# Performance work log

Measured on AMD Instinct MI355X. Metric: run time of the kernel, lower is better.

The kernel has to match this reference:

```python
import jax, jax.numpy as jnp
import numpy as np

BASE_R = 0.1      # base_radius (compared against squared distances)
K = 20            # PositionEncoder k
H = 0.1           # dilated_ball_query bandwidth
EPS_BN = 1e-5


def _gelu(x):
    return jax.nn.gelu(x, approximate=False)  # torch nn.GELU default (erf)


def _bn(x, g, b):
    # eval-mode BatchNorm (running_mean=0, running_var=1), channel axis = 1
    shape = (1, -1) + (1,) * (x.ndim - 2)
    scale = g / np.float32(np.sqrt(1.0 + EPS_BN))
    return x * scale.reshape(shape) + b.reshape(shape)


def _conv1x1(x, w):
    # pointwise conv (no bias): w [out_c, in_c], x [B, in_c, ...]
    return jnp.einsum('oc,bc...->bo...', w, x)


def _l1norm(x, axis):
    # F.normalize(p=1): divide by L1 norm clamped to 1e-12
    return x / jnp.maximum(jnp.sum(jnp.abs(x), axis=axis, keepdims=True), 1e-12)


def _forward(xyz, w_q, g_q, b_q, w_k, g_k, b_k, w_v, g_v, b_v,
             w_pe, b_pe, g_pe, bb_pe, w_m1, g_m1, b_m1, w_m2, g_m2, b_m2,
             w_out, g_out, b_out):
    B, _, N = xyz.shape
    # ---- pairwise squared distances [B,N,N] ----
    sq = jnp.sum(xyz * xyz, axis=1)
    dist = -2.0 * jnp.einsum('bcn,bcm->bnm', xyz, xyz) + sq[:, :, None] + sq[:, None, :]
    # ---- dilated ball query (sigma=1) ----
    gauss = jnp.exp(-dist / (2.0 * H * H))
    kd = jnp.sum(gauss, axis=-1, keepdims=True)                 # [B,N,1]
    kd_score = kd / (jnp.max(kd, axis=1, keepdims=True) + 1e-9)
    radius = BASE_R + BASE_R * kd_score                         # max_radius = 2*base
    keep = dist < radius                                        # [B,N,N]
    # ---- masked attention (emb_cent == emb_x == cat(xyz, xyz)) ----
    emb = jnp.concatenate([xyz, xyz], axis=1)                   # [B,6,N]
    q = _bn(_conv1x1(emb, w_q), g_q, b_q)                       # [B,1,N]
    k_ = _bn(_conv1x1(emb, w_k), g_k, b_k)                      # [B,1,N]
    scores = jnp.einsum('bhn,bhm->bnm', q, k_)                  # [B,N,N]
    scores = jnp.where(keep, scores, -1e9)
    adj = jax.nn.softmax(scores, axis=-1)
    adj = _l1norm(_l1norm(adj, 1), -1)                          # doubly L1-normalized
    # ---- graph smoothing + value conv ----
    smoothed = jnp.einsum('bcn,bnm->bcm', xyz, adj)
    variation = smoothed - xyz
    v = _bn(_conv1x1(jnp.concatenate([variation, xyz], axis=1), w_v), g_v, b_v)  # [B,64,N]
    # ---- position encoder: ball-query top-k neighbor gather ----
    ar = jnp.arange(N, dtype=jnp.int32)[None, None, :]
    idx = jnp.where(dist > radius, N, ar)                       # mark out-of-ball with N
    idx = jnp.sort(idx, axis=-1)[:, :, :K]                      # k nearest-index in-ball
    idx = jnp.where(idx == N, idx[:, :, :1], idx)               # pad with first neighbor
    grouped = jax.vmap(lambda f, i: f[:, i])(xyz, idx)          # [B,3,N,K]
    pts = jnp.broadcast_to(xyz[:, :, :, None], grouped.shape)
    pf = jnp.concatenate([pts, grouped, grouped - pts], axis=1)  # [B,9,N,K]
    pf = _conv1x1(pf, w_pe) + b_pe[None, :, None, None]          # conv2d 1x1 with bias
    pf = _gelu(_bn(pf, g_pe, bb_pe))
    pf = jnp.max(pf, axis=-1)                                    # [B,out/8,N]
    pf = _gelu(_bn(_conv1x1(pf, w_m1), g_m1, b_m1))              # [B,out/4,N]
    pos = _bn(_conv1x1(pf, w_m2), g_m2, b_m2)                    # [B,out,N]
    out = _gelu(v + pos)
    return _bn(_conv1x1(out, w_out), g_out, b_out)               # [B,32,N]


def setup_inputs() -> dict:
    key = jax.random.key(0)
    ks = iter(jax.random.split(key, 40))
    B, N, OC = 4, 4096, 64

    def w(shape):
        return jax.random.normal(next(ks), shape, jnp.float32) / np.float32(np.sqrt(shape[-1]))

    def gb(c):
        g = 1.0 + 0.1 * jax.random.normal(next(ks), (c,), jnp.float32)
        b = 0.1 * jax.random.normal(next(ks), (c,), jnp.float32)
        return g, b

    xyz = jax.random.uniform(next(ks), (B, 3, N), jnp.float32)
    g_q, b_q = gb(1)
    g_k, b_k = gb(1)
    g_v, b_v = gb(OC)
    g_pe, bb_pe = gb(OC // 8)
    g_m1, b_m1 = gb(OC // 4)
    g_m2, b_m2 = gb(OC)
    g_out, b_out = gb(32)
    return {
        'xyz': xyz,
        'w_q': w((1, 6)), 'g_q': g_q, 'b_q': b_q,
        'w_k': w((1, 6)), 'g_k': g_k, 'b_k': b_k,
        'w_v': w((OC, 6)), 'g_v': g_v, 'b_v': b_v,
        'w_pe': w((OC // 8, 9)), 'b_pe': 0.1 * jax.random.normal(next(ks), (OC // 8,), jnp.float32),
        'g_pe': g_pe, 'bb_pe': bb_pe,
        'w_m1': w((OC // 4, OC // 8)), 'g_m1': g_m1, 'b_m1': b_m1,
        'w_m2': w((OC, OC // 4)), 'g_m2': g_m2, 'b_m2': b_m2,
        'w_out': w((32, OC)), 'g_out': g_out, 'b_out': b_out,
    }


def reference(xyz, w_q, g_q, b_q, w_k, g_k, b_k, w_v, g_v, b_v,
              w_pe, b_pe, g_pe, bb_pe, w_m1, g_m1, b_m1, w_m2, g_m2, b_m2,
              w_out, g_out, b_out):
    return _forward(xyz, w_q, g_q, b_q, w_k, g_k, b_k, w_v, g_v, b_v,
                    w_pe, b_pe, g_pe, bb_pe, w_m1, g_m1, b_m1, w_m2, g_m2, b_m2,
                    w_out, g_out, b_out)
```

## Files before the change

kernel.cpp:

```cpp
#include <hip/hip_runtime.h>
#include <math.h>

#define BB 4
#define NN 4096
#define KNBR 20
#define BN (BB * NN)
#define HALF 2048
#define RPW 128

__device__ __forceinline__ float gelu_f(float x) {
    return 0.5f * x * (1.0f + erff(x * 0.70710678118654752440f));
}

__global__ void k0_prep(const float* __restrict__ xyz,
                        const float* __restrict__ w_q, const float* __restrict__ g_q, const float* __restrict__ b_q,
                        const float* __restrict__ w_k, const float* __restrict__ g_k, const float* __restrict__ b_k,
                        float* __restrict__ qv, float* __restrict__ kv, float4* __restrict__ pts4) {
    int t = blockIdx.x * blockDim.x + threadIdx.x;
    if (t >= BN) return;
    int b = t / NN, n = t % NN;
    const float* base = xyz + (size_t)b * 3 * NN;
    float x = base[n], y = base[NN + n], z = base[2 * NN + n];
    float sq = x * x + y * y + z * z;
    const float invs = rsqrtf(1.0f + 1e-5f);
    float qr = x * (w_q[0] + w_q[3]) + y * (w_q[1] + w_q[4]) + z * (w_q[2] + w_q[5]);
    float kr = x * (w_k[0] + w_k[3]) + y * (w_k[1] + w_k[4]) + z * (w_k[2] + w_k[5]);
    qv[t] = qr * (g_q[0] * invs) + b_q[0];
    kv[t] = kr * (g_k[0] * invs) + b_k[0];
    pts4[t] = make_float4(x, y, z, sq);
}

__global__ __launch_bounds__(1024, 8)
void p1_kd(const float4* __restrict__ pts4, float* __restrict__ part) {
    int tid = threadIdx.x;
    int wave = __builtin_amdgcn_readfirstlane(tid >> 6);
    int lane = tid & 63;
    int g = blockIdx.x >> 1, half = blockIdx.x & 1;
    int b = g >> 6;
    const float4* p = pts4 + (size_t)b * NN;
    float4 fr = pts4[g * 64 + lane];
    float acc = 0.f;
    int i0 = half * HALF + wave * RPW;
    for (int i = i0; i < i0 + RPW; i += 8) {
        float4 fc[8];
        #pragma unroll
        for (int u = 0; u < 8; ++u) fc[u] = p[i + u];
        #pragma unroll
        for (int u = 0; u < 8; ++u) {
            float dot = fr.x * fc[u].x + fr.y * fc[u].y + fr.z * fc[u].z;
            float d = fmaf(-2.0f, dot, fr.w) + fc[u].w;
            acc += __expf(-50.0f * d);
        }
    }
    __shared__ float s_red[16][64];
    s_red[wave][lane] = acc;
    __syncthreads();
    if (tid < 64) {
        float s = 0.f;
        #pragma unroll
        for (int w = 0; w < 16; ++w) s += s_red[w][tid];
        part[half * BN + g * 64 + tid] = s;
    }
}

__global__ void k2_radius(const float* __restrict__ part, const float4* __restrict__ pts4,
                          const float* __restrict__ qv, const float* __restrict__ kv,
                          float* __restrict__ radius, float4* __restrict__ recB) {
    int b = blockIdx.x;
    int t = threadIdx.x;
    float kdv[4];
    float mx = -1e30f;
    #pragma unroll
    for (int j = 0; j < 4; ++j) {
        int n = b * NN + j * 1024 + t;
        kdv[j] = part[n] + part[BN + n];
        mx = fmaxf(mx, kdv[j]);
    }
    __shared__ float red[1024];
    red[t] = mx;
    __syncthreads();
    for (int s = 512; s > 0; s >>= 1) {
        if (t < s) red[t] = fmaxf(red[t], red[t + s]);
        __syncthreads();
    }
    float kmax = red[0];
    #pragma unroll
    for (int j = 0; j < 4; ++j) {
        int n = b * NN + j * 1024 + t;
        float rad = 0.1f + 0.1f * (kdv[j] / (kmax + 1e-9f));
        radius[n] = rad;
        recB[2 * n] = pts4[n];
        recB[2 * n + 1] = make_float4(kv[n], qv[n], rad, 0.f);
    }
}

__global__ __launch_bounds__(1024, 8)
void p3_Zk7(const float4* __restrict__ recB, const float4* __restrict__ pts4,
            const float* __restrict__ radius, float* __restrict__ part,
            int* __restrict__ idxg) {
    int tid = threadIdx.x;
    int wave = __builtin_amdgcn_readfirstlane(tid >> 6);
    int lane = tid & 63;
    int g = blockIdx.x >> 1, half = blockIdx.x & 1;
    int b = g >> 6;
    const float4* rb = recB + (size_t)b * NN * 2;
    int row = g * 64 + lane;
    float4 fr = recB[2 * row];
    float4 rowa = recB[2 * row + 1];
    float qn = rowa.y, rad = rowa.z;
    float acc = 0.f;
    int i0 = half * HALF + wave * RPW;
    for (int i = i0; i < i0 + RPW; i += 8) {
        float4 fc[8], an[8];
        #pragma unroll
        for (int u = 0; u < 8; ++u) {
            fc[u] = rb[2 * (i + u)];
            an[u] = rb[2 * (i + u) + 1];
        }
        #pragma unroll
        for (int u = 0; u < 8; ++u) {
            float dot = fr.x * fc[u].x + fr.y * fc[u].y + fr.z * fc[u].z;
            float d = fmaf(-2.0f, dot, fr.w) + fc[u].w;
            float e = __expf(qn * an[u].x);
            acc += (d < rad) ? e : 0.f;
        }
    }
    __shared__ float s_red[16][64];
    s_red[wave][lane] = acc;
    __syncthreads();
    if (tid < 64) {
        float s = 0.f;
        #pragma unroll
        for (int w = 0; w < 16; ++w) s += s_red[w][tid];
        part[half * BN + g * 64 + tid] = s;
    }
    int gw = blockIdx.x * 16 + wave;
    for (int rr = 0; rr < 2; ++rr) {
        int row7 = gw * 2 + rr;
        int b7 = row7 / NN;
        const float4* p7 = pts4 + (size_t)b7 * NN;
        float4 f7 = pts4[row7];
        float rad7 = radius[row7];
        int total = 0, firstm = 0;
        bool have = false;
        unsigned long long lmask = (1ULL << lane) - 1ULL;
        for (int i = 0; i < NN / 64 && total < KNBR; ++i) {
            int m = i * 64 + lane;
            float4 fc = p7[m];
            float dot = f7.x * fc.x + f7.y * fc.y + f7.z * fc.z;
            float d = fmaf(-2.0f, dot, f7.w) + fc.w;
            bool inb = !(d > rad7);
            unsigned long long mask = __ballot(inb);
            if (!have && mask != 0ULL) {
                int src = __ffsll(mask) - 1;
                firstm = __shfl(m, src);
                have = true;
            }
            int pos = total + (int)__popcll(mask & lmask);
            if (inb && pos < KNBR) idxg[(size_t)row7 * KNBR + pos] = m;
            total += (int)__popcll(mask);
        }
        if (total < KNBR && lane >= total && lane < KNBR)
            idxg[(size_t)row7 * KNBR + lane] = firstm;
    }
}

__global__ void r3_Z(const float* __restrict__ part, const float4* __restrict__ pts4,
                     const float* __restrict__ qv, const float* __restrict__ radius,
                     float* __restrict__ Z, float4* __restrict__ recC) {
    int t = blockIdx.x * blockDim.x + threadIdx.x;
    float s = part[t] + part[BN + t];
    Z[t] = s;
    recC[2 * t] = pts4[t];
    recC[2 * t + 1] = make_float4(qv[t], radius[t], __logf(s), 0.f);
}

__global__ __launch_bounds__(1024, 8)
void p4_colsum(const float4* __restrict__ recC, const float4* __restrict__ recB,
               float* __restrict__ part) {
    int tid = threadIdx.x;
    int wave = __builtin_amdgcn_readfirstlane(tid >> 6);
    int lane = tid & 63;
    int g = blockIdx.x >> 1, half = blockIdx.x & 1;
    int b = g >> 6;
    const float4* rc = recC + (size_t)b * NN * 2;
    int col = g * 64 + lane;
    float4 fcc = recB[2 * col];
    float km = recB[2 * col + 1].x;
    float acc = 0.f;
    int i0 = half * HALF + wave * RPW;
    for (int i = i0; i < i0 + RPW; i += 8) {
        float4 fr[8], an[8];
        #pragma unroll
        for (int u = 0; u < 8; ++u) {
            fr[u] = rc[2 * (i + u)];
            an[u] = rc[2 * (i + u) + 1];
        }
        #pragma unroll
        for (int u = 0; u < 8; ++u) {
            float dot = fr[u].x * fcc.x + fr[u].y * fcc.y + fr[u].z * fcc.z;
            float d = fmaf(-2.0f, dot, fr[u].w) + fcc.w;
            float e = __expf(an[u].x * km - an[u].z);
            acc += (d < an[u].y) ? e : 0.f;
        }
    }
    __shared__ float s_red[16][64];
    s_red[wave][lane] = acc;
    __syncthreads();
    if (tid < 64) {
        float s = 0.f;
        #pragma unroll
        for (int w = 0; w < 16; ++w) s += s_red[w][tid];
        part[half * BN + g * 64 + tid] = s;
    }
}

__global__ void r4_colsum(const float* __restrict__ part, const float4* __restrict__ pts4,
                          const float* __restrict__ kv, float* __restrict__ colsum,
                          float4* __restrict__ recD) {
    int t = blockIdx.x * blockDim.x + threadIdx.x;
    float s = fmaxf(part[t] + part[BN + t], 1e-12f);
    colsum[t] = s;
    recD[2 * t] = pts4[t];
    recD[2 * t + 1] = make_float4(kv[t], __logf(s), 0.f, 0.f);
}

__global__ __launch_bounds__(1024, 8)
void p5_rs(const float4* __restrict__ recD, const float4* __restrict__ recB,
           float* __restrict__ part) {
    int tid = threadIdx.x;
    int wave = __builtin_amdgcn_readfirstlane(tid >> 6);
    int lane = tid & 63;
    int g = blockIdx.x >> 1, half = blockIdx.x & 1;
    int b = g >> 6;
    const float4* rd = recD + (size_t)b * NN * 2;
    int row = g * 64 + lane;
    float4 fr = recB[2 * row];
    float4 rowa = recB[2 * row + 1];
    float qn = rowa.y, rad = rowa.z;
    float acc = 0.f;
    int i0 = half * HALF + wave * RPW;
    for (int i = i0; i < i0 + RPW; i += 8) {
        float4 fc[8], an[8];
        #pragma unroll
        for (int u = 0; u < 8; ++u) {
            fc[u] = rd[2 * (i + u)];
            an[u] = rd[2 * (i + u) + 1];
        }
        #pragma unroll
        for (int u = 0; u < 8; ++u) {
            float dot = fr.x * fc[u].x + fr.y * fc[u].y + fr.z * fc[u].z;
            float d = fmaf(-2.0f, dot, fr.w) + fc[u].w;
            float e = __expf(qn * an[u].x - an[u].y);
            acc += (d < rad) ? e : 0.f;
        }
    }
    __shared__ float s_red[16][64];
    s_red[wave][lane] = acc;
    __syncthreads();
    if (tid < 64) {
        float s = 0.f;
        #pragma unroll
        for (int w = 0; w < 16; ++w) s += s_red[w][tid];
        part[half * BN + g * 64 + tid] = s;
    }
}

__global__ void r5_rs(const float* __restrict__ part, const float* __restrict__ Z,
                      const float4* __restrict__ recC, const float4* __restrict__ pts4,
                      float4* __restrict__ recE) {
    int t = blockIdx.x * blockDim.x + threadIdx.x;
    float s = part[t] + part[BN + t];
    float rs = fmaxf(s / Z[t], 1e-12f);
    float4 a = recC[2 * t + 1];
    recE[2 * t] = pts4[t];
    recE[2 * t + 1] = make_float4(a.x, a.y, a.z + __logf(rs), 0.f);
}

__global__ __launch_bounds__(1024, 8)
void p6_smooth(const float4* __restrict__ recE, const float4* __restrict__ recB,
               float* __restrict__ partx, float* __restrict__ party,
               float* __restrict__ partz) {
    int tid = threadIdx.x;
    int wave = __builtin_amdgcn_readfirstlane(tid >> 6);
    int lane = tid & 63;
    int g = blockIdx.x >> 1, half = blockIdx.x & 1;
    int b = g >> 6;
    const float4* re = recE + (size_t)b * NN * 2;
    int col = g * 64 + lane;
    float4 fcc = recB[2 * col];
    float km = recB[2 * col + 1].x;
    float ax = 0.f, ay = 0.f, az = 0.f;
    int i0 = half * HALF + wave * RPW;
    for (int i = i0; i < i0 + RPW; i += 8) {
        float4 fr[8], an[8];
        #pragma unroll
        for (int u = 0; u < 8; ++u) {
            fr[u] = re[2 * (i + u)];
            an[u] = re[2 * (i + u) + 1];
        }
        #pragma unroll
        for (int u = 0; u < 8; ++u) {
            float dot = fr[u].x * fcc.x + fr[u].y * fcc.y + fr[u].z * fcc.z;
            float d = fmaf(-2.0f, dot, fr[u].w) + fcc.w;
            float w = __expf(an[u].x * km - an[u].z);
            w = (d < an[u].y) ? w : 0.f;
            ax += fr[u].x * w;
            ay += fr[u].y * w;
            az += fr[u].z * w;
        }
    }
    __shared__ float s_rx[16][64];
    __shared__ float s_ry[16][64];
    __shared__ float s_rz[16][64];
    s_rx[wave][lane] = ax;
    s_ry[wave][lane] = ay;
    s_rz[wave][lane] = az;
    __syncthreads();
    if (tid < 64) {
        float sx = 0.f, sy = 0.f, sz = 0.f;
        #pragma unroll
        for (int w = 0; w < 16; ++w) {
            sx += s_rx[w][tid];
            sy += s_ry[w][tid];
            sz += s_rz[w][tid];
        }
        int o = half * BN + g * 64 + tid;
        partx[o] = sx;
        party[o] = sy;
        partz[o] = sz;
    }
}

__global__ void k8_final(const float* __restrict__ xyz,
                         const float* __restrict__ partx, const float* __restrict__ party,
                         const float* __restrict__ partz, const float* __restrict__ colsum,
                         const int* __restrict__ idxg,
                         const float* __restrict__ w_v, const float* __restrict__ g_v, const float* __restrict__ b_v,
                         const float* __restrict__ w_pe, const float* __restrict__ b_pe,
                         const float* __restrict__ g_pe, const float* __restrict__ bb_pe,
                         const float* __restrict__ w_m1, const float* __restrict__ g_m1, const float* __restrict__ b_m1,
                         const float* __restrict__ w_m2, const float* __restrict__ g_m2, const float* __restrict__ b_m2,
                         const float* __restrict__ w_out, const float* __restrict__ g_out, const float* __restrict__ b_out,
                         float* __restrict__ out) {
    __shared__ float s_pf8[32][9];
    __shared__ float s_pf16[32][17];
    __shared__ float s_g64[32][65];
    int tid = threadIdx.x;
    int ptL = tid >> 3, o = tid & 7;
    int p = blockIdx.x * 32 + ptL;
    int b = p / NN, n = p % NN;
    const float* xb = xyz + (size_t)b * 3 * NN;
    float x = xb[n], y = xb[NN + n], z = xb[2 * NN + n];
    const float invs = rsqrtf(1.0f + 1e-5f);

    float w0 = w_pe[o * 9 + 0], w1 = w_pe[o * 9 + 1], w2 = w_pe[o * 9 + 2];
    float w3 = w_pe[o * 9 + 3], w4 = w_pe[o * 9 + 4], w5 = w_pe[o * 9 + 5];
    float w6 = w_pe[o * 9 + 6], w7 = w_pe[o * 9 + 7], w8 = w_pe[o * 9 + 8];
    float bp = b_pe[o], gp = g_pe[o] * invs, bbp = bb_pe[o];
    float mx = -1e30f;
    for (int kk = 0; kk < KNBR; ++kk) {
        int j = idxg[(size_t)p * KNBR + kk];
        float gx = xb[j], gy = xb[NN + j], gz = xb[2 * NN + j];
        float dx = gx - x, dy = gy - y, dz = gz - z;
        float s = w0 * x + w1 * y + w2 * z + w3 * gx + w4 * gy + w5 * gz
                + w6 * dx + w7 * dy + w8 * dz + bp;
        s = gelu_f(s * gp + bbp);
        mx = fmaxf(mx, s);
    }
    s_pf8[ptL][o] = mx;
    __syncthreads();

    #pragma unroll
    for (int rr = 0; rr < 2; ++rr) {
        int r = o + rr * 8;
        const float* w = w_m1 + r * 8;
        float s = 0.f;
        #pragma unroll
        for (int c = 0; c < 8; ++c) s += w[c] * s_pf8[ptL][c];
        s_pf16[ptL][r] = gelu_f(s * (g_m1[r] * invs) + b_m1[r]);
    }
    __syncthreads();

    float inv = 1.0f / colsum[p];
    float vx = (partx[p] + partx[BN + p]) * inv - x;
    float vy = (party[p] + party[BN + p]) * inv - y;
    float vz = (partz[p] + partz[BN + p]) * inv - z;
    #pragma unroll
    for (int i = 0; i < 8; ++i) {
        int ch = o * 8 + i;
        const float* wm = w_m2 + ch * 16;
        float pos = 0.f;
        #pragma unroll
        for (int c = 0; c < 16; ++c) pos += wm[c] * s_pf16[ptL][c];
        pos = pos * (g_m2[ch] * invs) + b_m2[ch];
        const float* wv = w_v + ch * 6;
        float vv = wv[0] * vx + wv[1] * vy + wv[2] * vz + wv[3] * x + wv[4] * y + wv[5] * z;
        vv = vv * (g_v[ch] * invs) + b_v[ch];
        s_g64[ptL][ch] = gelu_f(vv + pos);
    }
    __syncthreads();

    #pragma unroll
    for (int i = 0; i < 4; ++i) {
        int ch = o * 4 + i;
        const float* w = w_out + ch * 64;
        float s = 0.f;
        #pragma unroll
        for (int c = 0; c < 64; ++c) s += w[c] * s_g64[ptL][c];
        out[((size_t)b * 32 + ch) * NN + n] = s * (g_out[ch] * invs) + b_out[ch];
    }
}

extern "C" void kernel_launch(void* const* d_in, const int* in_sizes, int n_in,
                              void* d_out, int out_size, void* d_ws, size_t ws_size,
                              hipStream_t stream) {
    const float* xyz  = (const float*)d_in[0];
    const float* w_q  = (const float*)d_in[1];
    const float* g_q  = (const float*)d_in[2];
    const float* b_q  = (const float*)d_in[3];
    const float* w_k  = (const float*)d_in[4];
    const float* g_k  = (const float*)d_in[5];
    const float* b_k  = (const float*)d_in[6];
    const float* w_v  = (const float*)d_in[7];
    const float* g_v  = (const float*)d_in[8];
    const float* b_v  = (const float*)d_in[9];
    const float* w_pe = (const float*)d_in[10];
    const float* b_pe = (const float*)d_in[11];
    const float* g_pe = (const float*)d_in[12];
    const float* bb_pe= (const float*)d_in[13];
    const float* w_m1 = (const float*)d_in[14];
    const float* g_m1 = (const float*)d_in[15];
    const float* b_m1 = (const float*)d_in[16];
    const float* w_m2 = (const float*)d_in[17];
    const float* g_m2 = (const float*)d_in[18];
    const float* b_m2 = (const float*)d_in[19];
    const float* w_out= (const float*)d_in[20];
    const float* g_out= (const float*)d_in[21];
    const float* b_out= (const float*)d_in[22];

    float* ws = (float*)d_ws;
    float*  qv     = ws;
    float*  kv     = ws + (size_t)1  * BN;
    float4* pts4   = (float4*)(ws + (size_t)2  * BN);
    float*  radius = ws + (size_t)6  * BN;
    float*  Zv     = ws + (size_t)7  * BN;
    float*  colsum = ws + (size_t)8  * BN;
    float4* recB   = (float4*)(ws + (size_t)9  * BN);
    float4* recC   = (float4*)(ws + (size_t)17 * BN);
    float4* recD   = (float4*)(ws + (size_t)25 * BN);
    float4* recE   = (float4*)(ws + (size_t)33 * BN);
    int*    idxg   = (int*)   (ws + (size_t)41 * BN);
    float*  part1  = ws + (size_t)61 * BN;
    float*  part3  = ws + (size_t)63 * BN;
    float*  part5  = ws + (size_t)65 * BN;
    float*  part7  = ws + (size_t)67 * BN;
    float*  partx  = ws + (size_t)69 * BN;
    float*  party  = ws + (size_t)71 * BN;
    float*  partz  = ws + (size_t)73 * BN;

    const int PB = (BN / 64) * 2;

    k0_prep<<<BN / 256, 256, 0, stream>>>(xyz, w_q, g_q, b_q, w_k, g_k, b_k, qv, kv, pts4);
    p1_kd<<<PB, 1024, 0, stream>>>(pts4, part1);
    k2_radius<<<BB, 1024, 0, stream>>>(part1, pts4, qv, kv, radius, recB);
    p3_Zk7<<<PB, 1024, 0, stream>>>(recB, pts4, radius, part3, idxg);
    r3_Z<<<BN / 256, 256, 0, stream>>>(part3, pts4, qv, radius, Zv, recC);
    p4_colsum<<<PB, 1024, 0, stream>>>(recC, recB, part5);
    r4_colsum<<<BN / 256, 256, 0, stream>>>(part5, pts4, kv, colsum, recD);
    p5_rs<<<PB, 1024, 0, stream>>>(recD, recB, part7);
    r5_rs<<<BN / 256, 256, 0, stream>>>(part7, Zv, recC, pts4, recE);
    p6_smooth<<<PB, 1024, 0, stream>>>(recE, recB, partx, party, partz);
    k8_final<<<BN / 32, 256, 0, stream>>>(xyz, partx, party, partz, colsum, idxg,
                                          w_v, g_v, b_v,
                                          w_pe, b_pe, g_pe, bb_pe,
                                          w_m1, g_m1, b_m1,
                                          w_m2, g_m2, b_m2,
                                          w_out, g_out, b_out,
                                          (float*)d_out);
}
```

Baseline: 280.6 us.

## Stage column tiles in LDS with register prefetch across pairwise kernels

Each of the five O(N^2) pairwise kernels now cooperatively loads a 1024-float4 chunk of the half-range into shared memory, with the next chunk prefetched into registers, and each wave reads its slice from LDS. Before, every wave issued its own uniform global loads per iteration. The aim is to replace per-wave global/scalar loads with one coalesced block load plus LDS broadcast reads. In exchange it adds barriers per chunk and 16KB of LDS per block, which may reduce occupancy.

```diff
diff --git a/kernel.cpp b/kernel.cpp
--- a/kernel.cpp
+++ b/kernel.cpp
@@ -6,7 +6,6 @@
 #define KNBR 20
 #define BN (BB * NN)
 #define HALF 2048
-#define RPW 128
 
 __device__ __forceinline__ float gelu_f(float x) {
     return 0.5f * x * (1.0f + erff(x * 0.70710678118654752440f));
@@ -32,27 +31,31 @@
 
 __global__ __launch_bounds__(1024, 8)
 void p1_kd(const float4* __restrict__ pts4, float* __restrict__ part) {
+    __shared__ float4 stg[1024];
+    __shared__ float s_red[16][64];
     int tid = threadIdx.x;
     int wave = __builtin_amdgcn_readfirstlane(tid >> 6);
     int lane = tid & 63;
     int g = blockIdx.x >> 1, half = blockIdx.x & 1;
     int b = g >> 6;
-    const float4* p = pts4 + (size_t)b * NN;
+    const float4* src = pts4 + (size_t)b * NN + (size_t)half * HALF;
     float4 fr = pts4[g * 64 + lane];
     float acc = 0.f;
-    int i0 = half * HALF + wave * RPW;
-    for (int i = i0; i < i0 + RPW; i += 8) {
-        float4 fc[8];
-        #pragma unroll
-        for (int u = 0; u < 8; ++u) fc[u] = p[i + u];
-        #pragma unroll
-        for (int u = 0; u < 8; ++u) {
-            float dot = fr.x * fc[u].x + fr.y * fc[u].y + fr.z * fc[u].z;
-            float d = fmaf(-2.0f, dot, fr.w) + fc[u].w;
+    float4 pre = src[tid];
+    for (int c = 0; c < 2; ++c) {
+        __syncthreads();
+        stg[tid] = pre;
+        __syncthreads();
+        if (c < 1) pre = src[1024 + tid];
+        int j0 = wave * 64;
+        #pragma unroll 8
+        for (int j = j0; j < j0 + 64; ++j) {
+            float4 fc = stg[j];
+            float dot = fr.x * fc.x + fr.y * fc.y + fr.z * fc.z;
+            float d = fmaf(-2.0f, dot, fr.w) + fc.w;
             acc += __expf(-50.0f * d);
         }
     }
-    __shared__ float s_red[16][64];
     s_red[wave][lane] = acc;
     __syncthreads();
     if (tid < 64) {
@@ -98,34 +101,36 @@
 void p3_Zk7(const float4* __restrict__ recB, const float4* __restrict__ pts4,
             const float* __restrict__ radius, float* __restrict__ part,
             int* __restrict__ idxg) {
+    __shared__ float4 stg[1024];
+    __shared__ float s_red[16][64];
     int tid = threadIdx.x;
     int wave = __builtin_amdgcn_readfirstlane(tid >> 6);
     int lane = tid & 63;
     int g = blockIdx.x >> 1, half = blockIdx.x & 1;
     int b = g >> 6;
-    const float4* rb = recB + (size_t)b * NN * 2;
+    const float4* src = recB + ((size_t)b * NN + (size_t)half * HALF) * 2;
     int row = g * 64 + lane;
     float4 fr = recB[2 * row];
     float4 rowa = recB[2 * row + 1];
     float qn = rowa.y, rad = rowa.z;
     float acc = 0.f;
-    int i0 = half * HALF + wave * RPW;
-    for (int i = i0; i < i0 + RPW; i += 8) {
-        float4 fc[8], an[8];
-        #pragma unroll
-        for (int u = 0; u < 8; ++u) {
-            fc[u] = rb[2 * (i + u)];
-            an[u] = rb[2 * (i + u) + 1];
-        }
-        #pragma unroll
-        for (int u = 0; u < 8; ++u) {
-            float dot = fr.x * fc[u].x + fr.y * fc[u].y + fr.z * fc[u].z;
-            float d = fmaf(-2.0f, dot, fr.w) + fc[u].w;
-            float e = __expf(qn * an[u].x);
+    float4 pre = src[tid];
+    for (int c = 0; c < 4; ++c) {
+        __syncthreads();
+        stg[tid] = pre;
+        __syncthreads();
+        if (c < 3) pre = src[(c + 1) * 1024 + tid];
+        int j0 = wave * 32;
+        #pragma unroll 8
+        for (int j = j0; j < j0 + 32; ++j) {
+            float4 fc = stg[2 * j];
+            float4 an = stg[2 * j + 1];
+            float dot = fr.x * fc.x + fr.y * fc.y + fr.z * fc.z;
+            float d = fmaf(-2.0f, dot, fr.w) + fc.w;
+            float e = __expf(qn * an.x);
             acc += (d < rad) ? e : 0.f;
         }
     }
-    __shared__ float s_red[16][64];
     s_red[wave][lane] = acc;
     __syncthreads();
     if (tid < 64) {
@@ -152,8 +157,8 @@
             bool inb = !(d > rad7);
             unsigned long long mask = __ballot(inb);
             if (!have && mask != 0ULL) {
-                int src = __ffsll(mask) - 1;
-                firstm = __shfl(m, src);
+                int src7 = __ffsll(mask) - 1;
+                firstm = __shfl(m, src7);
                 have = true;
             }
             int pos = total + (int)__popcll(mask & lmask);
@@ -178,33 +183,35 @@
 __global__ __launch_bounds__(1024, 8)
 void p4_colsum(const float4* __restrict__ recC, const float4* __restrict__ recB,
                float* __restrict__ part) {
+    __shared__ float4 stg[1024];
+    __shared__ float s_red[16][64];
     int tid = threadIdx.x;
     int wave = __builtin_amdgcn_readfirstlane(tid >> 6);
     int lane = tid & 63;
     int g = blockIdx.x >> 1, half = blockIdx.x & 1;
     int b = g >> 6;
-    const float4* rc = recC + (size_t)b * NN * 2;
+    const float4* src = recC + ((size_t)b * NN + (size_t)half * HALF) * 2;
     int col = g * 64 + lane;
     float4 fcc = recB[2 * col];
     float km = recB[2 * col + 1].x;
     float acc = 0.f;
-    int i0 = half * HALF + wave * RPW;
-    for (int i = i0; i < i0 + RPW; i += 8) {
-        float4 fr[8], an[8];
-        #pragma unroll
-        for (int u = 0; u < 8; ++u) {
-            fr[u] = rc[2 * (i + u)];
-            an[u] = rc[2 * (i + u) + 1];
-        }
-        #pragma unroll
-        for (int u = 0; u < 8; ++u) {
-            float dot = fr[u].x * fcc.x + fr[u].y * fcc.y + fr[u].z * fcc.z;
-            float d = fmaf(-2.0f, dot, fr[u].w) + fcc.w;
-            float e = __expf(an[u].x * km - an[u].z);
-            acc += (d < an[u].y) ? e : 0.f;
-        }
-    }
-    __shared__ float s_red[16][64];
+    float4 pre = src[tid];
+    for (int c = 0; c < 4; ++c) {
+        __syncthreads();
+        stg[tid] = pre;
+        __syncthreads();
+        if (c < 3) pre = src[(c + 1) * 1024 + tid];
+        int j0 = wave * 32;
+        #pragma unroll 8
+        for (int j = j0; j < j0 + 32; ++j) {
+            float4 fr = stg[2 * j];
+            float4 an = stg[2 * j + 1];
+            float dot = fr.x * fcc.x + fr.y * fcc.y + fr.z * fcc.z;
+            float d = fmaf(-2.0f, dot, fr.w) + fcc.w;
+            float e = __expf(an.x * km - an.z);
+            acc += (d < an.y) ? e : 0.f;
+        }
+    }
     s_red[wave][lane] = acc;
     __syncthreads();
     if (tid < 64) {
@@ -228,34 +235,36 @@
 __global__ __launch_bounds__(1024, 8)
 void p5_rs(const float4* __restrict__ recD, const float4* __restrict__ recB,
            float* __restrict__ part) {
+    __shared__ float4 stg[1024];
+    __shared__ float s_red[16][64];
     int tid = threadIdx.x;
     int wave = __builtin_amdgcn_readfirstlane(tid >> 6);
     int lane = tid & 63;
     int g = blockIdx.x >> 1, half = blockIdx.x & 1;
     int b = g >> 6;
-    const float4* rd = recD + (size_t)b * NN * 2;
+    const float4* src = recD + ((size_t)b * NN + (size_t)half * HALF) * 2;
     int row = g * 64 + lane;
     float4 fr = recB[2 * row];
     float4 rowa = recB[2 * row + 1];
     float qn = rowa.y, rad = rowa.z;
     float acc = 0.f;
-    int i0 = half * HALF + wave * RPW;
-    for (int i = i0; i < i0 + RPW; i += 8) {
-        float4 fc[8], an[8];
-        #pragma unroll
-        for (int u = 0; u < 8; ++u) {
-            fc[u] = rd[2 * (i + u)];
-            an[u] = rd[2 * (i + u) + 1];
-        }
-        #pragma unroll
-        for (int u = 0; u < 8; ++u) {
-            float dot = fr.x * fc[u].x + fr.y * fc[u].y + fr.z * fc[u].z;
-            float d = fmaf(-2.0f, dot, fr.w) + fc[u].w;
-            float e = __expf(qn * an[u].x - an[u].y);
+    float4 pre = src[tid];
+    for (int c = 0; c < 4; ++c) {
+        __syncthreads();
+        stg[tid] = pre;
+        __syncthreads();
+        if (c < 3) pre = src[(c + 1) * 1024 + tid];
+        int j0 = wave * 32;
+        #pragma unroll 8
+        for (int j = j0; j < j0 + 32; ++j) {
+            float4 fc = stg[2 * j];
+            float4 an = stg[2 * j + 1];
+            float dot = fr.x * fc.x + fr.y * fc.y + fr.z * fc.z;
+            float d = fmaf(-2.0f, dot, fr.w) + fc.w;
+            float e = __expf(qn * an.x - an.y);
             acc += (d < rad) ? e : 0.f;
         }
     }
-    __shared__ float s_red[16][64];
     s_red[wave][lane] = acc;
     __syncthreads();
     if (tid < 64) {
@@ -281,38 +290,40 @@
 void p6_smooth(const float4* __restrict__ recE, const float4* __restrict__ recB,
                float* __restrict__ partx, float* __restrict__ party,
                float* __restrict__ partz) {
+    __shared__ float4 stg[1024];
+    __shared__ float s_rx[16][64];
+    __shared__ float s_ry[16][64];
+    __shared__ float s_rz[16][64];
     int tid = threadIdx.x;
     int wave = __builtin_amdgcn_readfirstlane(tid >> 6);
     int lane = tid & 63;
     int g = blockIdx.x >> 1, half = blockIdx.x & 1;
     int b = g >> 6;
-    const float4* re = recE + (size_t)b * NN * 2;
+    const float4* src = recE + ((size_t)b * NN + (size_t)half * HALF) * 2;
     int col = g * 64 + lane;
     float4 fcc = recB[2 * col];
     float km = recB[2 * col + 1].x;
     float ax = 0.f, ay = 0.f, az = 0.f;
-    int i0 = half * HALF + wave * RPW;
-    for (int i = i0; i < i0 + RPW; i += 8) {
-        float4 fr[8], an[8];
-        #pragma unroll
-        for (int u = 0; u < 8; ++u) {
-            fr[u] = re[2 * (i + u)];
-            an[u] = re[2 * (i + u) + 1];
-        }
-        #pragma unroll
-        for (int u = 0; u < 8; ++u) {
-            float dot = fr[u].x * fcc.x + fr[u].y * fcc.y + fr[u].z * fcc.z;
-            float d = fmaf(-2.0f, dot, fr[u].w) + fcc.w;
-            float w = __expf(an[u].x * km - an[u].z);
-            w = (d < an[u].y) ? w : 0.f;
-            ax += fr[u].x * w;
-            ay += fr[u].y * w;
-            az += fr[u].z * w;
-        }
-    }
-    __shared__ float s_rx[16][64];
-    __shared__ float s_ry[16][64];
-    __shared__ float s_rz[16][64];
+    float4 pre = src[tid];
+    for (int c = 0; c < 4; ++c) {
+        __syncthreads();
+        stg[tid] = pre;
+        __syncthreads();
+        if (c < 3) pre = src[(c + 1) * 1024 + tid];
+        int j0 = wave * 32;
+        #pragma unroll 8
+        for (int j = j0; j < j0 + 32; ++j) {
+            float4 fr = stg[2 * j];
+            float4 an = stg[2 * j + 1];
+            float dot = fr.x * fcc.x + fr.y * fcc.y + fr.z * fcc.z;
+            float d = fmaf(-2.0f, dot, fr.w) + fcc.w;
+            float w = __expf(an.x * km - an.z);
+            w = (d < an.y) ? w : 0.f;
+            ax += fr.x * w;
+            ay += fr.y * w;
+            az += fr.z * w;
+        }
+    }
     s_rx[wave][lane] = ax;
     s_ry[wave][lane] = ay;
     s_rz[wave][lane] = az;
```

Measured after the change: 289.8 us. +3.3%, slower.

## Register-tile four rows per thread and split columns into eight slices

Applied to the files above, without the earlier changes.

Each thread now accumulates four rows (or columns) in registers while streaming one shared column record per iteration, across all five pairwise passes. Each fetched record is therefore reused four times instead of once, cutting per-pair load traffic. To keep the block count unchanged, the column range is split into eight slices instead of two. The per-point reductions now sum eight partial buffers, which needs more workspace and adds extra reads in the reduce kernels.

```diff
diff --git a/kernel.cpp b/kernel.cpp
--- a/kernel.cpp
+++ b/kernel.cpp
@@ -5,8 +5,9 @@
 #define NN 4096
 #define KNBR 20
 #define BN (BB * NN)
-#define HALF 2048
-#define RPW 128
+#define NSLICE 8
+#define SLEN (NN / NSLICE)
+#define JPW (SLEN / 16)
 
 __device__ __forceinline__ float gelu_f(float x) {
     return 0.5f * x * (1.0f + erff(x * 0.70710678118654752440f));
@@ -30,36 +31,38 @@
     pts4[t] = make_float4(x, y, z, sq);
 }
 
+
 __global__ __launch_bounds__(1024, 8)
 void p1_kd(const float4* __restrict__ pts4, float* __restrict__ part) {
+    __shared__ float s_red[16][256];
     int tid = threadIdx.x;
     int wave = __builtin_amdgcn_readfirstlane(tid >> 6);
     int lane = tid & 63;
-    int g = blockIdx.x >> 1, half = blockIdx.x & 1;
-    int b = g >> 6;
-    const float4* p = pts4 + (size_t)b * NN;
-    float4 fr = pts4[g * 64 + lane];
-    float acc = 0.f;
-    int i0 = half * HALF + wave * RPW;
-    for (int i = i0; i < i0 + RPW; i += 8) {
-        float4 fc[8];
-        #pragma unroll
-        for (int u = 0; u < 8; ++u) fc[u] = p[i + u];
-        #pragma unroll
-        for (int u = 0; u < 8; ++u) {
-            float dot = fr.x * fc[u].x + fr.y * fc[u].y + fr.z * fc[u].z;
-            float d = fmaf(-2.0f, dot, fr.w) + fc[u].w;
-            acc += __expf(-50.0f * d);
-        }
-    }
-    __shared__ float s_red[16][64];
-    s_red[wave][lane] = acc;
-    __syncthreads();
-    if (tid < 64) {
+    int g = blockIdx.x >> 3, slice = blockIdx.x & 7;
+    int b = g >> 4;
+    const float4* rb = pts4 + (size_t)b * NN + slice * SLEN + wave * JPW;
+    float4 fr[4];
+    float acc[4] = {0.f, 0.f, 0.f, 0.f};
+    #pragma unroll
+    for (int rr = 0; rr < 4; ++rr) fr[rr] = pts4[g * 256 + rr * 64 + lane];
+    #pragma unroll 4
+    for (int j = 0; j < JPW; ++j) {
+        float4 fc = rb[j];
+        #pragma unroll
+        for (int rr = 0; rr < 4; ++rr) {
+            float dot = fr[rr].x * fc.x + fr[rr].y * fc.y + fr[rr].z * fc.z;
+            float d = fmaf(-2.0f, dot, fr[rr].w) + fc.w;
+            acc[rr] += __expf(-50.0f * d);
+        }
+    }
+    #pragma unroll
+    for (int rr = 0; rr < 4; ++rr) s_red[wave][rr * 64 + lane] = acc[rr];
+    __syncthreads();
+    if (tid < 256) {
         float s = 0.f;
         #pragma unroll
         for (int w = 0; w < 16; ++w) s += s_red[w][tid];
-        part[half * BN + g * 64 + tid] = s;
+        part[slice * BN + g * 256 + tid] = s;
     }
 }
 
@@ -73,8 +76,11 @@
     #pragma unroll
     for (int j = 0; j < 4; ++j) {
         int n = b * NN + j * 1024 + t;
-        kdv[j] = part[n] + part[BN + n];
-        mx = fmaxf(mx, kdv[j]);
+        float s = 0.f;
+        #pragma unroll
+        for (int c = 0; c < NSLICE; ++c) s += part[c * BN + n];
+        kdv[j] = s;
+        mx = fmaxf(mx, s);
     }
     __shared__ float red[1024];
     red[t] = mx;
@@ -98,41 +104,44 @@
 void p3_Zk7(const float4* __restrict__ recB, const float4* __restrict__ pts4,
             const float* __restrict__ radius, float* __restrict__ part,
             int* __restrict__ idxg) {
+    __shared__ float s_red[16][256];
     int tid = threadIdx.x;
     int wave = __builtin_amdgcn_readfirstlane(tid >> 6);
     int lane = tid & 63;
-    int g = blockIdx.x >> 1, half = blockIdx.x & 1;
-    int b = g >> 6;
-    const float4* rb = recB + (size_t)b * NN * 2;
-    int row = g * 64 + lane;
-    float4 fr = recB[2 * row];
-    float4 rowa = recB[2 * row + 1];
-    float qn = rowa.y, rad = rowa.z;
-    float acc = 0.f;
-    int i0 = half * HALF + wave * RPW;
-    for (int i = i0; i < i0 + RPW; i += 8) {
-        float4 fc[8], an[8];
-        #pragma unroll
-        for (int u = 0; u < 8; ++u) {
-            fc[u] = rb[2 * (i + u)];
-            an[u] = rb[2 * (i + u) + 1];
-        }
-        #pragma unroll
-        for (int u = 0; u < 8; ++u) {
-            float dot = fr.x * fc[u].x + fr.y * fc[u].y + fr.z * fc[u].z;
-            float d = fmaf(-2.0f, dot, fr.w) + fc[u].w;
-            float e = __expf(qn * an[u].x);
-            acc += (d < rad) ? e : 0.f;
-        }
-    }
-    __shared__ float s_red[16][64];
-    s_red[wave][lane] = acc;
-    __syncthreads();
-    if (tid < 64) {
+    int g = blockIdx.x >> 3, slice = blockIdx.x & 7;
+    int b = g >> 4;
+    const float4* rb = recB + ((size_t)b * NN + slice * SLEN + wave * JPW) * 2;
+    float4 fr[4];
+    float q[4], rad[4];
+    float acc[4] = {0.f, 0.f, 0.f, 0.f};
+    #pragma unroll
+    for (int rr = 0; rr < 4; ++rr) {
+        int r = g * 256 + rr * 64 + lane;
+        fr[rr] = recB[2 * r];
+        float4 a = recB[2 * r + 1];
+        q[rr] = a.y;
+        rad[rr] = a.z;
+    }
+    #pragma unroll 4
+    for (int j = 0; j < JPW; ++j) {
+        float4 fc = rb[2 * j];
+        float4 an = rb[2 * j + 1];
+        #pragma unroll
+        for (int rr = 0; rr < 4; ++rr) {
+            float dot = fr[rr].x * fc.x + fr[rr].y * fc.y + fr[rr].z * fc.z;
+            float d = fmaf(-2.0f, dot, fr[rr].w) + fc.w;
+            float e = __expf(q[rr] * an.x);
+            acc[rr] += (d < rad[rr]) ? e : 0.f;
+        }
+    }
+    #pragma unroll
+    for (int rr = 0; rr < 4; ++rr) s_red[wave][rr * 64 + lane] = acc[rr];
+    __syncthreads();
+    if (tid < 256) {
         float s = 0.f;
         #pragma unroll
         for (int w = 0; w < 16; ++w) s += s_red[w][tid];
-        part[half * BN + g * 64 + tid] = s;
+        part[slice * BN + g * 256 + tid] = s;
     }
     int gw = blockIdx.x * 16 + wave;
     for (int rr = 0; rr < 2; ++rr) {
@@ -152,8 +161,8 @@
             bool inb = !(d > rad7);
             unsigned long long mask = __ballot(inb);
             if (!have && mask != 0ULL) {
-                int src = __ffsll(mask) - 1;
-                firstm = __shfl(m, src);
+                int src7 = __ffsll(mask) - 1;
+                firstm = __shfl(m, src7);
                 have = true;
             }
             int pos = total + (int)__popcll(mask & lmask);
@@ -169,7 +178,9 @@
                      const float* __restrict__ qv, const float* __restrict__ radius,
                      float* __restrict__ Z, float4* __restrict__ recC) {
     int t = blockIdx.x * blockDim.x + threadIdx.x;
-    float s = part[t] + part[BN + t];
+    float s = 0.f;
+    #pragma unroll
+    for (int c = 0; c < NSLICE; ++c) s += part[c * BN + t];
     Z[t] = s;
     recC[2 * t] = pts4[t];
     recC[2 * t + 1] = make_float4(qv[t], radius[t], __logf(s), 0.f);
@@ -178,40 +189,42 @@
 __global__ __launch_bounds__(1024, 8)
 void p4_colsum(const float4* __restrict__ recC, const float4* __restrict__ recB,
                float* __restrict__ part) {
+    __shared__ float s_red[16][256];
     int tid = threadIdx.x;
     int wave = __builtin_amdgcn_readfirstlane(tid >> 6);
     int lane = tid & 63;
-    int g = blockIdx.x >> 1, half = blockIdx.x & 1;
-    int b = g >> 6;
-    const float4* rc = recC + (size_t)b * NN * 2;
-    int col = g * 64 + lane;
-    float4 fcc = recB[2 * col];
-    float km = recB[2 * col + 1].x;
-    float acc = 0.f;
-    int i0 = half * HALF + wave * RPW;
-    for (int i = i0; i < i0 + RPW; i += 8) {
-        float4 fr[8], an[8];
-        #pragma unroll
-        for (int u = 0; u < 8; ++u) {
-            fr[u] = rc[2 * (i + u)];
-            an[u] = rc[2 * (i + u) + 1];
-        }
-        #pragma unroll
-        for (int u = 0; u < 8; ++u) {
-            float dot = fr[u].x * fcc.x + fr[u].y * fcc.y + fr[u].z * fcc.z;
-            float d = fmaf(-2.0f, dot, fr[u].w) + fcc.w;
-            float e = __expf(an[u].x * km - an[u].z);
-            acc += (d < an[u].y) ? e : 0.f;
-        }
-    }
-    __shared__ float s_red[16][64];
-    s_red[wave][lane] = acc;
-    __syncthreads();
-    if (tid < 64) {
+    int g = blockIdx.x >> 3, slice = blockIdx.x & 7;
+    int b = g >> 4;
+    const float4* rb = recC + ((size_t)b * NN + slice * SLEN + wave * JPW) * 2;
+    float4 fcc[4];
+    float km[4];
+    float acc[4] = {0.f, 0.f, 0.f, 0.f};
+    #pragma unroll
+    for (int rr = 0; rr < 4; ++rr) {
+        int c = g * 256 + rr * 64 + lane;
+        fcc[rr] = recB[2 * c];
+        km[rr] = recB[2 * c + 1].x;
+    }
+    #pragma unroll 4
+    for (int j = 0; j < JPW; ++j) {
+        float4 fc = rb[2 * j];
+        float4 an = rb[2 * j + 1];
+        #pragma unroll
+        for (int rr = 0; rr < 4; ++rr) {
+            float dot = fc.x * fcc[rr].x + fc.y * fcc[rr].y + fc.z * fcc[rr].z;
+            float d = fmaf(-2.0f, dot, fc.w) + fcc[rr].w;
+            float e = __expf(an.x * km[rr] - an.z);
+            acc[rr] += (d < an.y) ? e : 0.f;
+        }
+    }
+    #pragma unroll
+    for (int rr = 0; rr < 4; ++rr) s_red[wave][rr * 64 + lane] = acc[rr];
+    __syncthreads();
+    if (tid < 256) {
         float s = 0.f;
         #pragma unroll
         for (int w = 0; w < 16; ++w) s += s_red[w][tid];
-        part[half * BN + g * 64 + tid] = s;
+        part[slice * BN + g * 256 + tid] = s;
     }
 }
 
@@ -219,7 +232,10 @@
                           const float* __restrict__ kv, float* __restrict__ colsum,
                           float4* __restrict__ recD) {
     int t = blockIdx.x * blockDim.x + threadIdx.x;
-    float s = fmaxf(part[t] + part[BN + t], 1e-12f);
+    float s = 0.f;
+    #pragma unroll
+    for (int c = 0; c < NSLICE; ++c) s += part[c * BN + t];
+    s = fmaxf(s, 1e-12f);
     colsum[t] = s;
     recD[2 * t] = pts4[t];
     recD[2 * t + 1] = make_float4(kv[t], __logf(s), 0.f, 0.f);
@@ -228,41 +244,44 @@
 __global__ __launch_bounds__(1024, 8)
 void p5_rs(const float4* __restrict__ recD, const float4* __restrict__ recB,
            float* __restrict__ part) {
+    __shared__ float s_red[16][256];
     int tid = threadIdx.x;
     int wave = __builtin_amdgcn_readfirstlane(tid >> 6);
     int lane = tid & 63;
-    int g = blockIdx.x >> 1, half = blockIdx.x & 1;
-    int b = g >> 6;
-    const float4* rd = recD + (size_t)b * NN * 2;
-    int row = g * 64 + lane;
-    float4 fr = recB[2 * row];
-    float4 rowa = recB[2 * row + 1];
-    float qn = rowa.y, rad = rowa.z;
-    float acc = 0.f;
-    int i0 = half * HALF + wave * RPW;
-    for (int i = i0; i < i0 + RPW; i += 8) {
-        float4 fc[8], an[8];
-        #pragma unroll
-        for (int u = 0; u < 8; ++u) {
-            fc[u] = rd[2 * (i + u)];
-            an[u] = rd[2 * (i + u) + 1];
-        }
-        #pragma unroll
-        for (int u = 0; u < 8; ++u) {
-            float dot = fr.x * fc[u].x + fr.y * fc[u].y + fr.z * fc[u].z;
-            float d = fmaf(-2.0f, dot, fr.w) + fc[u].w;
-            float e = __expf(qn * an[u].x - an[u].y);
-            acc += (d < rad) ? e : 0.f;
-        }
-    }
-    __shared__ float s_red[16][64];
-    s_red[wave][lane] = acc;
-    __syncthreads();
-    if (tid < 64) {
+    int g = blockIdx.x >> 3, slice = blockIdx.x & 7;
+    int b = g >> 4;
+    const float4* rb = recD + ((size_t)b * NN + slice * SLEN + wave * JPW) * 2;
+    float4 fr[4];
+    float q[4], rad[4];
+    float acc[4] = {0.f, 0.f, 0.f, 0.f};
+    #pragma unroll
+    for (int rr = 0; rr < 4; ++rr) {
+        int r = g * 256 + rr * 64 + lane;
+        fr[rr] = recB[2 * r];
+        float4 a = recB[2 * r + 1];
+        q[rr] = a.y;
+        rad[rr] = a.z;
+    }
+    #pragma unroll 4
+    for (int j = 0; j < JPW; ++j) {
+        float4 fc = rb[2 * j];
+        float4 an = rb[2 * j + 1];
+        #pragma unroll
+        for (int rr = 0; rr < 4; ++rr) {
+            float dot = fr[rr].x * fc.x + fr[rr].y * fc.y + fr[rr].z * fc.z;
+            float d = fmaf(-2.0f, dot, fr[rr].w) + fc.w;
+            float e = __expf(q[rr] * an.x - an.y);
+            acc[rr] += (d < rad[rr]) ? e : 0.f;
+        }
+    }
+    #pragma unroll
+    for (int rr = 0; rr < 4; ++rr) s_red[wave][rr * 64 + lane] = acc[rr];
+    __syncthreads();
+    if (tid < 256) {
         float s = 0.f;
         #pragma unroll
         for (int w = 0; w < 16; ++w) s += s_red[w][tid];
-        part[half * BN + g * 64 + tid] = s;
+        part[slice * BN + g * 256 + tid] = s;
     }
 }
 
@@ -270,7 +289,9 @@
                       const float4* __restrict__ recC, const float4* __restrict__ pts4,
                       float4* __restrict__ recE) {
     int t = blockIdx.x * blockDim.x + threadIdx.x;
-    float s = part[t] + part[BN + t];
+    float s = 0.f;
+    #pragma unroll
+    for (int c = 0; c < NSLICE; ++c) s += part[c * BN + t];
     float rs = fmaxf(s / Z[t], 1e-12f);
     float4 a = recC[2 * t + 1];
     recE[2 * t] = pts4[t];
@@ -281,43 +302,49 @@
 void p6_smooth(const float4* __restrict__ recE, const float4* __restrict__ recB,
                float* __restrict__ partx, float* __restrict__ party,
                float* __restrict__ partz) {
+    __shared__ float s_rx[16][256];
+    __shared__ float s_ry[16][256];
+    __shared__ float s_rz[16][256];
     int tid = threadIdx.x;
     int wave = __builtin_amdgcn_readfirstlane(tid >> 6);
     int lane = tid & 63;
-    int g = blockIdx.x >> 1, half = blockIdx.x & 1;
-    int b = g >> 6;
-    const float4* re = recE + (size_t)b * NN * 2;
-    int col = g * 64 + lane;
-    float4 fcc = recB[2 * col];
-    float km = recB[2 * col + 1].x;
-    float ax = 0.f, ay = 0.f, az = 0.f;
-    int i0 = half * HALF + wave * RPW;
-    for (int i = i0; i < i0 + RPW; i += 8) {
-        float4 fr[8], an[8];
-        #pragma unroll
-        for (int u = 0; u < 8; ++u) {
-            fr[u] = re[2 * (i + u)];
-            an[u] = re[2 * (i + u) + 1];
-        }
-        #pragma unroll
-        for (int u = 0; u < 8; ++u) {
-            float dot = fr[u].x * fcc.x + fr[u].y * fcc.y + fr[u].z * fcc.z;
-            float d = fmaf(-2.0f, dot, fr[u].w) + fcc.w;
-            float w = __expf(an[u].x * km - an[u].z);
-            w = (d < an[u].y) ? w : 0.f;
-            ax += fr[u].x * w;
-            ay += fr[u].y * w;
-            az += fr[u].z * w;
-        }
-    }
-    __shared__ float s_rx[16][64];
-    __shared__ float s_ry[16][64];
-    __shared__ float s_rz[16][64];
-    s_rx[wave][lane] = ax;
-    s_ry[wave][lane] = ay;
-    s_rz[wave][lane] = az;
-    __syncthreads();
-    if (tid < 64) {
+    int g = blockIdx.x >> 3, slice = blockIdx.x & 7;
+    int b = g >> 4;
+    const float4* rb = recE + ((size_t)b * NN + slice * SLEN + wave * JPW) * 2;
+    float4 fcc[4];
+    float km[4];
+    float ax[4] = {0.f, 0.f, 0.f, 0.f};
+    float ay[4] = {0.f, 0.f, 0.f, 0.f};
+    float az[4] = {0.f, 0.f, 0.f, 0.f};
+    #pragma unroll
+    for (int rr = 0; rr < 4; ++rr) {
+        int c = g * 256 + rr * 64 + lane;
+        fcc[rr] = recB[2 * c];
+        km[rr] = recB[2 * c + 1].x;
+    }
+    #pragma unroll 2
+    for (int j = 0; j < JPW; ++j) {
+        float4 fc = rb[2 * j];
+        float4 an = rb[2 * j + 1];
+        #pragma unroll
+        for (int rr = 0; rr < 4; ++rr) {
+            float dot = fc.x * fcc[rr].x + fc.y * fcc[rr].y + fc.z * fcc[rr].z;
+            float d = fmaf(-2.0f, dot, fc.w) + fcc[rr].w;
+            float w = __expf(an.x * km[rr] - an.z);
+            w = (d < an.y) ? w : 0.f;
+            ax[rr] += fc.x * w;
+            ay[rr] += fc.y * w;
+            az[rr] += fc.z * w;
+        }
+    }
+    #pragma unroll
+    for (int rr = 0; rr < 4; ++rr) {
+        s_rx[wave][rr * 64 + lane] = ax[rr];
+        s_ry[wave][rr * 64 + lane] = ay[rr];
+        s_rz[wave][rr * 64 + lane] = az[rr];
+    }
+    __syncthreads();
+    if (tid < 256) {
         float sx = 0.f, sy = 0.f, sz = 0.f;
         #pragma unroll
         for (int w = 0; w < 16; ++w) {
@@ -325,7 +352,7 @@
             sy += s_ry[w][tid];
             sz += s_rz[w][tid];
         }
-        int o = half * BN + g * 64 + tid;
+        int o = slice * BN + g * 256 + tid;
         partx[o] = sx;
         party[o] = sy;
         partz[o] = sz;
@@ -383,9 +410,14 @@
     __syncthreads();
 
     float inv = 1.0f / colsum[p];
-    float vx = (partx[p] + partx[BN + p]) * inv - x;
-    float vy = (party[p] + party[BN + p]) * inv - y;
-    float vz = (partz[p] + partz[BN + p]) * inv - z;
+    float sx = 0.f, sy = 0.f, sz = 0.f;
+    #pragma unroll
+    for (int c = 0; c < NSLICE; ++c) {
+        sx += partx[c * BN + p];
+        sy += party[c * BN + p];
+        sz += partz[c * BN + p];
+    }
+    float vx = sx * inv - x, vy = sy * inv - y, vz = sz * inv - z;
     #pragma unroll
     for (int i = 0; i < 8; ++i) {
         int ch = o * 8 + i;
@@ -452,14 +484,14 @@
     float4* recE   = (float4*)(ws + (size_t)33 * BN);
     int*    idxg   = (int*)   (ws + (size_t)41 * BN);
     float*  part1  = ws + (size_t)61 * BN;
-    float*  part3  = ws + (size_t)63 * BN;
-    float*  part5  = ws + (size_t)65 * BN;
-    float*  part7  = ws + (size_t)67 * BN;
-    float*  partx  = ws + (size_t)69 * BN;
-    float*  party  = ws + (size_t)71 * BN;
-    float*  partz  = ws + (size_t)73 * BN;
-
-    const int PB = (BN / 64) * 2;
+    float*  part3  = ws + (size_t)69 * BN;
+    float*  part5  = ws + (size_t)77 * BN;
+    float*  part7  = ws + (size_t)85 * BN;
+    float*  partx  = ws + (size_t)93 * BN;
+    float*  party  = ws + (size_t)101 * BN;
+    float*  partz  = ws + (size_t)109 * BN;
+
+    const int PB = (BN / 256) * NSLICE;
 
     k0_prep<<<BN / 256, 256, 0, stream>>>(xyz, w_q, g_q, b_q, w_k, g_k, b_k, qv, kv, pts4);
     p1_kd<<<PB, 1024, 0, stream>>>(pts4, part1);
```

New measurement: 251.6 us. 10.4% less time.
